# Optimization experiments

Measured on AMD Instinct MI355X. Metric: run time of the kernel, lower is better.

The kernel has to match this reference:

```python
import jax, jax.numpy as jnp
import numpy as np

L_K = 3  # conv kernel width l


def _conv1d_shared(x, w):
    """x: [B, C, L], w: [l]. out[b,c,i] = sum_j x[b,c,i+j]*w[j] (kernel shared over channels).
    Matches torch Conv1d class: bmm of [B,C,l] slices with [l,1] weight."""
    l = w.shape[0]
    Lo = x.shape[-1] - l + 1
    out = jnp.zeros(x.shape[:2] + (Lo,), dtype=x.dtype)
    for j in range(l):  # small fixed loop over kernel taps
        out = out + x[:, :, j:j + Lo] * w[j]
    return out


def setup_inputs() -> dict:
    key = jax.random.key(0)
    k1, k2, k3, k4, k5 = jax.random.split(key, 5)
    B, S, D, H = 8192, 30, 512, 1024
    return {
        "emb": jax.random.normal(k1, (B, S, D), dtype=jnp.float32),
        "w_long": jax.random.uniform(k2, (L_K,), dtype=jnp.float32),
        "w_mid": jax.random.uniform(k3, (L_K,), dtype=jnp.float32),
        "W1": jax.random.normal(k4, (H, 3 * D), dtype=jnp.float32) * 0.02,
        "W2": jax.random.normal(k5, (1, H), dtype=jnp.float32) * 0.02,
    }


def reference(emb, w_long, w_mid, W1, W2):
    # emb: [B, 30, D]
    x = jnp.swapaxes(emb, 1, 2)                 # [B, D, 30]
    vl = _conv1d_shared(x, w_long).max(axis=-1)  # conv len 28, maxpool(28) -> [B, D]
    xm = x[:, :, -7:]                            # last 7 steps
    vm = _conv1d_shared(xm, w_mid).max(axis=-1)  # conv len 5, maxpool(5) -> [B, D]
    vs = emb[:, -1, :]                           # [B, D]
    feature = jnp.concatenate([vl, vm, vs], axis=1)  # [B, 3D]
    hidden = jnp.tanh(feature @ W1.T)                # [B, H]
    out = hidden @ W2.T                              # [B, 1]
    return out[:, 0]
```

## Files before the change

### kernel.cpp

```cpp
#include <hip/hip_runtime.h>


#define B_   8192
#define S_   30
#define D_   512
#define H_   1024
#define K_   1536

typedef float nf4 __attribute__((ext_vector_type(4)));

__device__ inline unsigned short f2bf(float f) {
    unsigned int u = __float_as_uint(f);
    u += 0x7FFFu + ((u >> 16) & 1u);
    return (unsigned short)(u >> 16);
}

__device__ inline nf4 fmax4(nf4 a, nf4 b) {
    nf4 r;
    r.x = fmaxf(a.x, b.x); r.y = fmaxf(a.y, b.y);
    r.z = fmaxf(a.z, b.z); r.w = fmaxf(a.w, b.w);
    return r;
}

__device__ inline void store_bf4(unsigned short* p, nf4 v) {
    ushort4 o;
    o.x = f2bf(v.x); o.y = f2bf(v.y); o.z = f2bf(v.z); o.w = f2bf(v.w);
    *(ushort4*)p = o;
}

__device__ inline nf4 ntload4(const float* p) {
    return __builtin_nontemporal_load((const nf4*)p);
}

__device__ inline float fast_tanh(float x) {
    float cx = fminf(fmaxf(x, -15.f), 15.f);
    float e = __expf(2.f * cx);
    return (e - 1.f) / (e + 1.f);
}

__global__ __launch_bounds__(256) void feat_kernel(
    const float* __restrict__ emb, const float* __restrict__ wl,
    const float* __restrict__ wm, unsigned short* __restrict__ feat)
{
    int gid = blockIdx.x * 256 + threadIdx.x;
    int b   = gid >> 7;
    int c4  = (gid & 127) << 2;

    const float* base = emb + (size_t)b * (S_ * D_) + c4;
    const float l0 = wl[0], l1 = wl[1], l2 = wl[2];
    const float m0 = wm[0], m1 = wm[1], m2 = wm[2];

    nf4 e0 = ntload4(base + 0 * D_);
    nf4 e1 = ntload4(base + 1 * D_);
    nf4 vl = {-3.4e38f, -3.4e38f, -3.4e38f, -3.4e38f};
    nf4 vm = vl;

    #pragma unroll 4
    for (int i = 0; i < 28; ++i) {
        nf4 e2 = ntload4(base + (i + 2) * D_);
        nf4 cv = e0 * l0 + e1 * l1 + e2 * l2;
        vl = fmax4(vl, cv);
        if (i >= 23) {
            nf4 cm = e0 * m0 + e1 * m1 + e2 * m2;
            vm = fmax4(vm, cm);
        }
        e0 = e1; e1 = e2;
    }
    unsigned short* frow = feat + (size_t)b * K_;
    store_bf4(frow + c4,            vl);
    store_bf4(frow + D_ + c4,       vm);
    store_bf4(frow + 2 * D_ + c4,   e1);
}

__global__ __launch_bounds__(256) void w1conv_kernel(
    const float* __restrict__ W1, unsigned short* __restrict__ w1b)
{
    int gid = blockIdx.x * 256 + threadIdx.x;
    nf4 v = ((const nf4*)W1)[gid];
    ushort4 o;
    o.x = f2bf(v.x); o.y = f2bf(v.y); o.z = f2bf(v.z); o.w = f2bf(v.w);
    ((ushort4*)w1b)[gid] = o;
}


typedef __bf16 bf16x8 __attribute__((ext_vector_type(8)));
typedef float  f32x4  __attribute__((ext_vector_type(4)));

#define GL2LDS(gp, lp) __builtin_amdgcn_global_load_lds( \
    (const __attribute__((address_space(1))) void*)(gp), \
    (__attribute__((address_space(3))) void*)(lp), 16, 0, 0)

#define NT_ (K_ / 64)

__global__ __launch_bounds__(256) void gemm_kernel(
    const unsigned short* __restrict__ A,
    const unsigned short* __restrict__ Bm,
    const float* __restrict__ W2,
    float* __restrict__ out)
{
    __shared__ unsigned short As[2][128 * 64];
    __shared__ unsigned short Bs[2][128 * 64];

    const int tid  = threadIdx.x;

    const int lg   = (blockIdx.x & 7) * 64 + (blockIdx.x >> 3);
    const int bm   = (lg >> 3) * 128;
    const int bn   = (lg & 7) * 128;

    const int lane = tid & 63;
    const int wm   = (tid >> 6) >> 1;
    const int wn   = (tid >> 6) & 1;
    const int lrow = lane & 15;
    const int quad = lane >> 4;

    f32x4 acc[4][4] = {};

    int s_row[4], s_jof[4];
    #pragma unroll
    for (int jj = 0; jj < 4; ++jj) {
        int q = tid + jj * 256;
        s_row[jj] = q >> 3;
        s_jof[jj] = (((q & 7) ^ (s_row[jj] & 7)) * 8);
    }

    auto stage = [&](int buf, int kt) {
        const int ko = kt * 64;
        #pragma unroll
        for (int jj = 0; jj < 4; ++jj) {
            int q = tid + jj * 256;
            GL2LDS(A  + (size_t)(bm + s_row[jj]) * K_ + ko + s_jof[jj], &As[buf][q * 8]);
            GL2LDS(Bm + (size_t)(bn + s_row[jj]) * K_ + ko + s_jof[jj], &Bs[buf][q * 8]);
        }
    };

    stage(0, 0);
    __syncthreads();

    for (int kt = 0; kt < NT_; ++kt) {
        const int cur = kt & 1;
        if (kt + 1 < NT_) stage(cur ^ 1, kt + 1);

        #pragma unroll
        for (int kk = 0; kk < 2; ++kk) {
            bf16x8 af[4], bf[4];
            const int j = kk * 4 + quad;
            #pragma unroll
            for (int mi = 0; mi < 4; ++mi) {
                int r = wm * 64 + mi * 16 + lrow;
                af[mi] = *(const bf16x8*)&As[cur][r * 64 + ((j ^ (r & 7)) * 8)];
            }
            #pragma unroll
            for (int ni = 0; ni < 4; ++ni) {
                int r = wn * 64 + ni * 16 + lrow;
                bf[ni] = *(const bf16x8*)&Bs[cur][r * 64 + ((j ^ (r & 7)) * 8)];
            }
            #pragma unroll
            for (int mi = 0; mi < 4; ++mi)
                #pragma unroll
                for (int ni = 0; ni < 4; ++ni)
                    acc[mi][ni] = __builtin_amdgcn_mfma_f32_16x16x32_bf16(
                        af[mi], bf[ni], acc[mi][ni], 0, 0, 0);
        }

        __syncthreads();
    }

    float w2v[4];
    #pragma unroll
    for (int ni = 0; ni < 4; ++ni)
        w2v[ni] = W2[bn + wn * 64 + ni * 16 + lrow];

    #pragma unroll
    for (int mi = 0; mi < 4; ++mi) {
        #pragma unroll
        for (int r = 0; r < 4; ++r) {
            float s = 0.f;
            #pragma unroll
            for (int ni = 0; ni < 4; ++ni)
                s += fast_tanh(acc[mi][ni][r]) * w2v[ni];
            #pragma unroll
            for (int off = 1; off < 16; off <<= 1)
                s += __shfl_xor(s, off, 64);
            if (lrow == 0)
                atomicAdd(&out[bm + wm * 64 + mi * 16 + quad * 4 + r], s);
        }
    }
}

extern "C" void kernel_launch(void* const* d_in, const int* in_sizes, int n_in,
                              void* d_out, int out_size, void* d_ws, size_t ws_size,
                              hipStream_t stream) {
    const float* emb = (const float*)d_in[0];
    const float* wl  = (const float*)d_in[1];
    const float* wm  = (const float*)d_in[2];
    const float* W1  = (const float*)d_in[3];
    const float* W2  = (const float*)d_in[4];
    float* out = (float*)d_out;

    unsigned short* feat = (unsigned short*)d_ws;
    unsigned short* w1b  = feat + (size_t)B_ * K_;

    (void)hipMemsetAsync(out, 0, sizeof(float) * B_, stream);

    hipLaunchKernelGGL(feat_kernel, dim3(B_ * (D_ / 4) / 256), dim3(256), 0, stream,
                       emb, wl, wm, feat);
    hipLaunchKernelGGL(w1conv_kernel, dim3(H_ * K_ / 4 / 256), dim3(256), 0, stream,
                       W1, w1b);
    hipLaunchKernelGGL(gemm_kernel, dim3((B_ / 128) * (H_ / 128)), dim3(256), 0, stream,
                       feat, w1b, W2, out);
}
```

Measured before the change: 668.4 us.

## Merge prep kernels with output zeroing and use 8 waves per GEMM tile

The conv/feature kernel, the W1 bf16 conversion and the output memset are combined into one launch, with the block index deciding which job each block does. This removes two launches and the memset call. The GEMM keeps its 128x128 tile but now runs 512 threads, eight waves in a 2x4 layout with 64x32 subtiles each. This lowers per-wave accumulator registers and staging loads to raise occupancy and latency hiding, at the cost of more LDS fragment reloads per MFMA.

```diff
diff --git a/kernel.cpp b/kernel.cpp
--- a/kernel.cpp
+++ b/kernel.cpp
@@ -38,48 +38,57 @@
     return (e - 1.f) / (e + 1.f);
 }
 
-__global__ __launch_bounds__(256) void feat_kernel(
+#define FEAT_BLKS  (B_ * (D_ / 4) / 256)
+#define W1C_BLKS   (H_ * K_ / 4 / 256)
+#define ZERO_BLKS  (B_ / (256 * 4))
+
+__global__ __launch_bounds__(256) void prep_kernel(
     const float* __restrict__ emb, const float* __restrict__ wl,
-    const float* __restrict__ wm, unsigned short* __restrict__ feat)
+    const float* __restrict__ wm, const float* __restrict__ W1,
+    unsigned short* __restrict__ feat, unsigned short* __restrict__ w1b,
+    float* __restrict__ out)
 {
-    int gid = blockIdx.x * 256 + threadIdx.x;
-    int b   = gid >> 7;
-    int c4  = (gid & 127) << 2;
-
-    const float* base = emb + (size_t)b * (S_ * D_) + c4;
-    const float l0 = wl[0], l1 = wl[1], l2 = wl[2];
-    const float m0 = wm[0], m1 = wm[1], m2 = wm[2];
-
-    nf4 e0 = ntload4(base + 0 * D_);
-    nf4 e1 = ntload4(base + 1 * D_);
-    nf4 vl = {-3.4e38f, -3.4e38f, -3.4e38f, -3.4e38f};
-    nf4 vm = vl;
-
-    #pragma unroll 4
-    for (int i = 0; i < 28; ++i) {
-        nf4 e2 = ntload4(base + (i + 2) * D_);
-        nf4 cv = e0 * l0 + e1 * l1 + e2 * l2;
-        vl = fmax4(vl, cv);
-        if (i >= 23) {
-            nf4 cm = e0 * m0 + e1 * m1 + e2 * m2;
-            vm = fmax4(vm, cm);
-        }
-        e0 = e1; e1 = e2;
-    }
-    unsigned short* frow = feat + (size_t)b * K_;
-    store_bf4(frow + c4,            vl);
-    store_bf4(frow + D_ + c4,       vm);
-    store_bf4(frow + 2 * D_ + c4,   e1);
-}
-
-__global__ __launch_bounds__(256) void w1conv_kernel(
-    const float* __restrict__ W1, unsigned short* __restrict__ w1b)
-{
-    int gid = blockIdx.x * 256 + threadIdx.x;
-    nf4 v = ((const nf4*)W1)[gid];
-    ushort4 o;
-    o.x = f2bf(v.x); o.y = f2bf(v.y); o.z = f2bf(v.z); o.w = f2bf(v.w);
-    ((ushort4*)w1b)[gid] = o;
+    const int blk = blockIdx.x;
+
+    if (blk < FEAT_BLKS) {
+        int gid = blk * 256 + threadIdx.x;
+        int b   = gid >> 7;
+        int c4  = (gid & 127) << 2;
+
+        const float* base = emb + (size_t)b * (S_ * D_) + c4;
+        const float l0 = wl[0], l1 = wl[1], l2 = wl[2];
+        const float m0 = wm[0], m1 = wm[1], m2 = wm[2];
+
+        nf4 e0 = ntload4(base + 0 * D_);
+        nf4 e1 = ntload4(base + 1 * D_);
+        nf4 vl = {-3.4e38f, -3.4e38f, -3.4e38f, -3.4e38f};
+        nf4 vm = vl;
+
+        #pragma unroll 4
+        for (int i = 0; i < 28; ++i) {
+            nf4 e2 = ntload4(base + (i + 2) * D_);
+            nf4 cv = e0 * l0 + e1 * l1 + e2 * l2;
+            vl = fmax4(vl, cv);
+            if (i >= 23) {
+                nf4 cm = e0 * m0 + e1 * m1 + e2 * m2;
+                vm = fmax4(vm, cm);
+            }
+            e0 = e1; e1 = e2;
+        }
+        unsigned short* frow = feat + (size_t)b * K_;
+        store_bf4(frow + c4,            vl);
+        store_bf4(frow + D_ + c4,       vm);
+        store_bf4(frow + 2 * D_ + c4,   e1);
+    } else if (blk < FEAT_BLKS + W1C_BLKS) {
+        int gid = (blk - FEAT_BLKS) * 256 + threadIdx.x;
+        nf4 v = ((const nf4*)W1)[gid];
+        ushort4 o;
+        o.x = f2bf(v.x); o.y = f2bf(v.y); o.z = f2bf(v.z); o.w = f2bf(v.w);
+        ((ushort4*)w1b)[gid] = o;
+    } else {
+        int gid = (blk - FEAT_BLKS - W1C_BLKS) * 256 + threadIdx.x;
+        ((nf4*)out)[gid] = (nf4){0.f, 0.f, 0.f, 0.f};
+    }
 }
 
 
@@ -92,7 +101,7 @@
 
 #define NT_ (K_ / 64)
 
-__global__ __launch_bounds__(256) void gemm_kernel(
+__global__ __launch_bounds__(512) void gemm_kernel(
     const unsigned short* __restrict__ A,
     const unsigned short* __restrict__ Bm,
     const float* __restrict__ W2,
@@ -108,17 +117,18 @@
     const int bn   = (lg & 7) * 128;
 
     const int lane = tid & 63;
-    const int wm   = (tid >> 6) >> 1;
-    const int wn   = (tid >> 6) & 1;
+    const int wid  = tid >> 6;
+    const int wm   = wid >> 2;
+    const int wn   = wid & 3;
     const int lrow = lane & 15;
     const int quad = lane >> 4;
 
-    f32x4 acc[4][4] = {};
-
-    int s_row[4], s_jof[4];
+    f32x4 acc[4][2] = {};
+
+    int s_row[2], s_jof[2];
     #pragma unroll
-    for (int jj = 0; jj < 4; ++jj) {
-        int q = tid + jj * 256;
+    for (int jj = 0; jj < 2; ++jj) {
+        int q = tid + jj * 512;
         s_row[jj] = q >> 3;
         s_jof[jj] = (((q & 7) ^ (s_row[jj] & 7)) * 8);
     }
@@ -126,8 +136,8 @@
     auto stage = [&](int buf, int kt) {
         const int ko = kt * 64;
         #pragma unroll
-        for (int jj = 0; jj < 4; ++jj) {
-            int q = tid + jj * 256;
+        for (int jj = 0; jj < 2; ++jj) {
+            int q = tid + jj * 512;
             GL2LDS(A  + (size_t)(bm + s_row[jj]) * K_ + ko + s_jof[jj], &As[buf][q * 8]);
             GL2LDS(Bm + (size_t)(bn + s_row[jj]) * K_ + ko + s_jof[jj], &Bs[buf][q * 8]);
         }
@@ -142,7 +152,7 @@
 
         #pragma unroll
         for (int kk = 0; kk < 2; ++kk) {
-            bf16x8 af[4], bf[4];
+            bf16x8 af[4], bf[2];
             const int j = kk * 4 + quad;
             #pragma unroll
             for (int mi = 0; mi < 4; ++mi) {
@@ -150,14 +160,14 @@
                 af[mi] = *(const bf16x8*)&As[cur][r * 64 + ((j ^ (r & 7)) * 8)];
             }
             #pragma unroll
-            for (int ni = 0; ni < 4; ++ni) {
-                int r = wn * 64 + ni * 16 + lrow;
+            for (int ni = 0; ni < 2; ++ni) {
+                int r = wn * 32 + ni * 16 + lrow;
                 bf[ni] = *(const bf16x8*)&Bs[cur][r * 64 + ((j ^ (r & 7)) * 8)];
             }
             #pragma unroll
             for (int mi = 0; mi < 4; ++mi)
                 #pragma unroll
-                for (int ni = 0; ni < 4; ++ni)
+                for (int ni = 0; ni < 2; ++ni)
                     acc[mi][ni] = __builtin_amdgcn_mfma_f32_16x16x32_bf16(
                         af[mi], bf[ni], acc[mi][ni], 0, 0, 0);
         }
@@ -165,10 +175,10 @@
         __syncthreads();
     }
 
-    float w2v[4];
+    float w2v[2];
     #pragma unroll
-    for (int ni = 0; ni < 4; ++ni)
-        w2v[ni] = W2[bn + wn * 64 + ni * 16 + lrow];
+    for (int ni = 0; ni < 2; ++ni)
+        w2v[ni] = W2[bn + wn * 32 + ni * 16 + lrow];
 
     #pragma unroll
     for (int mi = 0; mi < 4; ++mi) {
@@ -176,7 +186,7 @@
         for (int r = 0; r < 4; ++r) {
             float s = 0.f;
             #pragma unroll
-            for (int ni = 0; ni < 4; ++ni)
+            for (int ni = 0; ni < 2; ++ni)
                 s += fast_tanh(acc[mi][ni][r]) * w2v[ni];
             #pragma unroll
             for (int off = 1; off < 16; off <<= 1)
@@ -200,12 +210,8 @@
     unsigned short* feat = (unsigned short*)d_ws;
     unsigned short* w1b  = feat + (size_t)B_ * K_;
 
-    (void)hipMemsetAsync(out, 0, sizeof(float) * B_, stream);
-
-    hipLaunchKernelGGL(feat_kernel, dim3(B_ * (D_ / 4) / 256), dim3(256), 0, stream,
-                       emb, wl, wm, feat);
-    hipLaunchKernelGGL(w1conv_kernel, dim3(H_ * K_ / 4 / 256), dim3(256), 0, stream,
-                       W1, w1b);
-    hipLaunchKernelGGL(gemm_kernel, dim3((B_ / 128) * (H_ / 128)), dim3(256), 0, stream,
+    hipLaunchKernelGGL(prep_kernel, dim3(FEAT_BLKS + W1C_BLKS + ZERO_BLKS),
+                       dim3(256), 0, stream, emb, wl, wm, W1, feat, w1b, out);
+    hipLaunchKernelGGL(gemm_kernel, dim3((B_ / 128) * (H_ / 128)), dim3(512), 0, stream,
                        feat, w1b, W2, out);
 }
```

Result: no change. 657.7 us (-1.6%).
